# Optimization experiments

Hardware: AMD Instinct MI355X
Metric: run time of the kernel (lower is better)

Reference implementation:

```python
import jax, jax.numpy as jnp
import numpy as np

B, L, D_MODEL = 2, 4096, 1024
D_INNER = 2048  # expand * d_model
D_CONV = 4


def setup_inputs() -> dict:
    key = jax.random.key(0)
    ks = jax.random.split(key, 7)
    return {
        "hidden_states": jax.random.normal(ks[0], (B, L, D_MODEL), jnp.float32),
        "W_in": jax.random.normal(ks[1], (2 * D_INNER, D_MODEL), jnp.float32) * 0.02,
        "conv_w": jax.random.normal(ks[2], (D_INNER, D_CONV), jnp.float32) * 0.1,
        "conv_b": jax.random.normal(ks[3], (D_INNER,), jnp.float32) * 0.1,
        "k_ssm": jax.random.normal(ks[4], (D_INNER, L), jnp.float32) * 0.02,  # materialized SSM kernel (channels=1)
        "D_skip": jax.random.normal(ks[5], (D_INNER,), jnp.float32),
        "W_out": jax.random.normal(ks[6], (D_MODEL, D_INNER), jnp.float32) * 0.02,
    }


def _silu(x):
    return x * jax.nn.sigmoid(x)


def reference(hidden_states, W_in, conv_w, conv_b, k_ssm, D_skip, W_out):
    Bq, Lq, _ = hidden_states.shape
    # in_proj (no bias): (B, L, d_model) -> (B, 2*d_inner, L)
    xz = jnp.einsum('bld,ed->bel', hidden_states, W_in)
    x, z = jnp.split(xz, 2, axis=1)  # each (B, d_inner, L)

    # causal depthwise conv1d (pad left d_conv-1) + SiLU (causal_conv1d_fn)
    xp = jnp.pad(x, ((0, 0), (0, 0), (D_CONV - 1, 0)))
    xc = conv_b[None, :, None]
    for j in range(D_CONV):
        xc = xc + conv_w[None, :, j, None] * xp[:, :, j:j + Lq]
    x = _silu(xc)

    # FFT long convolution (l_kernel = L, n = 2L), channels = 1
    n = 2 * Lq
    x_f = jnp.fft.rfft(x, n=n)            # (B, H, n//2+1) complex
    k_f = jnp.fft.rfft(k_ssm, n=n)        # (H, n//2+1)
    y = jnp.fft.irfft(x_f * k_f[None], n=n)[..., :Lq]  # (B, H, L)

    # D skip connection
    y = y + x * D_skip[None, :, None]

    # gating with SiLU(z)
    y = y * _silu(z)

    # out_proj (no bias): (B, H, L) -> (B, L, d_model)
    return jnp.einsum('bhl,dh->bld', y, W_out)
```

## Files before the change

### kernel.cpp

```cpp
#include <hip/hip_runtime.h>
#include <hip/hip_bf16.h>
#include <math.h>

#define B_SZ 2
#define L_SZ 4096
#define DM   1024
#define DI   2048
#define E_SZ 4096
#define DC   4

typedef unsigned short u16;
typedef __attribute__((ext_vector_type(8))) short short8;
typedef __attribute__((ext_vector_type(4))) float f32x4;

__device__ __forceinline__ float silu_f(float v) {
    return v / (1.0f + __expf(-v));
}

__device__ __forceinline__ void split_bf16(float x, u16& h, u16& l) {
    unsigned u  = __float_as_uint(x);
    unsigned hb = u & 0xFFFF0000u;
    h = (u16)(hb >> 16);
    float lf = x - __uint_as_float(hb);
    l = (u16)(__float_as_uint(lf) >> 16);
}
__device__ __forceinline__ float bf2f(u16 h) {
    return __uint_as_float(((unsigned)h) << 16);
}

__device__ __forceinline__ void gld_lds16(const u16* g, u16* l) {
    __builtin_amdgcn_global_load_lds(
        (const __attribute__((address_space(1))) unsigned int*)g,
        (__attribute__((address_space(3))) unsigned int*)l, 16, 0, 0);
}

__global__ __launch_bounds__(256) void pack_rm(
    const float* __restrict__ X, u16* __restrict__ H, u16* __restrict__ Lo,
    int ldx, int r16n, long sX, long sOut)
{
    const long cid = (long)blockIdx.x * 256 + threadIdx.x;
    const int  qc  = (int)(cid & 63);
    const long blk = cid >> 6;
    const int  r16 = (int)(blk % r16n);
    const int  k32 = (int)(blk / r16n);
    const int  q = qc >> 4, m = qc & 15;

    const float* src = X + blockIdx.y * sX + (long)(r16 * 16 + m) * ldx + k32 * 32 + q * 8;
    float4 v0 = *(const float4*)src;
    float4 v1 = *(const float4*)(src + 4);
    float v[8] = {v0.x,v0.y,v0.z,v0.w,v1.x,v1.y,v1.z,v1.w};

    u16 hs[8], ls[8];
    #pragma unroll
    for (int j = 0; j < 8; ++j) split_bf16(v[j], hs[j], ls[j]);

    const long o = blockIdx.y * sOut + cid * 8;
    *(uint4*)&H[o]  = *(const uint4*)hs;
    *(uint4*)&Lo[o] = *(const uint4*)ls;
}

__global__ __launch_bounds__(256) void gemm_mfma(
    const u16* __restrict__ Ah, const u16* __restrict__ Al,
    const u16* __restrict__ Bh, const u16* __restrict__ Bl,
    float* __restrict__ C,
    int r16A, int r16B, long sA, long sB, long sC,
    int ldc, int nk32)
{
    __shared__ alignas(16) u16 sm[4][4096];

    const int tid  = threadIdx.x;
    const int wv   = tid >> 6, lane = tid & 63;
    const long zb  = blockIdx.z;

    const u16* srcs0 = Ah + zb * sA;
    const u16* srcs1 = Al + zb * sA;
    const u16* srcs2 = Bh + zb * sB;
    const u16* srcs3 = Bl + zb * sB;
    const u16* mysrc = (wv == 0) ? srcs0 : (wv == 1) ? srcs1 : (wv == 2) ? srcs2 : srcs3;
    const int  rblk  = (wv < 2) ? blockIdx.x * 8 : blockIdx.y * 8;
    const int  r16c  = (wv < 2) ? r16A : r16B;
    u16* myl = sm[wv];

    const int wr = wv >> 1, wc = wv & 1;

    f32x4 acc[4][4];
    #pragma unroll
    for (int i = 0; i < 4; ++i)
        #pragma unroll
        for (int j = 0; j < 4; ++j)
            #pragma unroll
            for (int r = 0; r < 4; ++r) acc[i][j][r] = 0.f;

    for (int s = 0; s < nk32; ++s) {
        if (s) __syncthreads();
        {
            const u16* g = mysrc + (((long)s * r16c + rblk) << 9) + lane * 8;
            #pragma unroll
            for (int i = 0; i < 8; ++i)
                gld_lds16(g + (i << 9), myl + (i << 9));
        }
        __syncthreads();

        short8 afh[4], afl[4], bfh[4], bfl[4];
        const int aoff = (wr * 4) * 512 + lane * 8;
        const int boff = (wc * 4) * 512 + lane * 8;
        #pragma unroll
        for (int t = 0; t < 4; ++t) {
            afh[t] = *(const short8*)&sm[0][aoff + t * 512];
            afl[t] = *(const short8*)&sm[1][aoff + t * 512];
            bfh[t] = *(const short8*)&sm[2][boff + t * 512];
            bfl[t] = *(const short8*)&sm[3][boff + t * 512];
        }
        #pragma unroll
        for (int i = 0; i < 4; ++i)
            #pragma unroll
            for (int j = 0; j < 4; ++j) {
                acc[i][j] = __builtin_amdgcn_mfma_f32_16x16x32_bf16(afh[i], bfh[j], acc[i][j], 0, 0, 0);
                acc[i][j] = __builtin_amdgcn_mfma_f32_16x16x32_bf16(afh[i], bfl[j], acc[i][j], 0, 0, 0);
                acc[i][j] = __builtin_amdgcn_mfma_f32_16x16x32_bf16(afl[i], bfh[j], acc[i][j], 0, 0, 0);
            }
    }

    const int m_ = lane & 15, q_ = lane >> 4;
    float* Cb = C + zb * sC;
    const int row00 = blockIdx.x * 128 + wr * 64 + q_ * 4;
    const int col0  = blockIdx.y * 128 + wc * 64 + m_;
    #pragma unroll
    for (int i = 0; i < 4; ++i)
        #pragma unroll
        for (int j = 0; j < 4; ++j) {
            const long base = (long)(row00 + i * 16) * ldc + col0 + j * 16;
            #pragma unroll
            for (int r = 0; r < 4; ++r)
                Cb[base + (long)r * ldc] = acc[i][j][r];
        }
}

__global__ __launch_bounds__(256) void conv_silu_split(
    const float* __restrict__ xz, const float* __restrict__ conv_w,
    const float* __restrict__ conv_b,
    u16* __restrict__ xh_gl, u16* __restrict__ xl_gl)
{
    const long gid = (long)blockIdx.x * 256 + threadIdx.x;
    const int  q   = (int)(gid % (L_SZ / 4));
    const long bc  = gid / (L_SZ / 4);
    const int  ch  = (int)(bc % DI);
    const int  b   = (int)(bc / DI);

    const float* row = xz + ((long)b * E_SZ + ch) * L_SZ;
    const int l0 = q * 4;

    float4 cur  = *(const float4*)&row[l0];
    float4 prev = q ? *(const float4*)&row[l0 - 4] : make_float4(0.f, 0.f, 0.f, 0.f);

    const float w0 = conv_w[ch*DC+0], w1 = conv_w[ch*DC+1];
    const float w2 = conv_w[ch*DC+2], w3 = conv_w[ch*DC+3];
    const float bias = conv_b[ch];

    float o[4];
    o[0] = silu_f(bias + w0*prev.y + w1*prev.z + w2*prev.w + w3*cur.x);
    o[1] = silu_f(bias + w0*prev.z + w1*prev.w + w2*cur.x  + w3*cur.y);
    o[2] = silu_f(bias + w0*prev.w + w1*cur.x  + w2*cur.y  + w3*cur.z);
    o[3] = silu_f(bias + w0*cur.x  + w1*cur.y  + w2*cur.z  + w3*cur.w);

    unsigned long long hp = 0ull, lp = 0ull;
    #pragma unroll
    for (int r = 0; r < 4; ++r) {
        u16 h, l; split_bf16(o[r], h, l);
        hp |= ((unsigned long long)h) << (16*r);
        lp |= ((unsigned long long)l) << (16*r);
    }
    const long base = ((long)b * DI + ch) * L_SZ + l0;
    *(unsigned long long*)&xh_gl[base] = hp;
    *(unsigned long long*)&xl_gl[base] = lp;
}

__global__ __launch_bounds__(256, 4) void longconv_mfma(
    u16* __restrict__ xh_gl, u16* __restrict__ xl_gl,
    const float* __restrict__ xz,  const float* __restrict__ k_ssm,
    const float* __restrict__ D_skip)
{
    __shared__ u16 XH[4352];
    __shared__ u16 XL[4352];

    const int tid  = threadIdx.x;
    const int lane = tid & 63;
    const int wv   = tid >> 6;
    const int wc   = blockIdx.x;
    const int ch   = wc & (DI - 1);
    const int b    = wc >> 11;

    u16*         xhr  = xh_gl + ((long)b * DI + ch) * L_SZ;
    u16*         xlr  = xl_gl + ((long)b * DI + ch) * L_SZ;
    const float* krow = k_ssm + (long)ch * L_SZ;

    if (tid < 64) {
        uint4 z = make_uint4(0u, 0u, 0u, 0u);
        ((uint4*)((tid < 32) ? XH : XL))[tid & 31] = z;
    }
    #pragma unroll
    for (int it = 0; it < 2; ++it) {
        const int idx = it * 256 + tid;
        *(uint4*)&XH[256 + idx * 8] = ((const uint4*)xhr)[idx];
        *(uint4*)&XL[256 + idx * 8] = ((const uint4*)xlr)[idx];
    }
    __syncthreads();

    const int m_ = lane & 15;
    const int q_ = lane >> 4;
    const int dq = m_ - 8 * q_ + ((q_ >= 2) ? 32 : 0);
    const int xoff_lane = 256 + 16 * m_ + 8 * q_ - ((q_ >= 2) ? 32 : 0);

    const int tset[4] = { wv, 7 - wv, 8 + wv, 15 - wv };
    const int tmax = 15 - wv;
    const int cmax = 8 * tmax + 7;

    f32x4 acc[4];
    #pragma unroll
    for (int u = 0; u < 4; ++u)
        #pragma unroll
        for (int r = 0; r < 4; ++r) acc[u][r] = 0.f;

    float kn[8];
    #pragma unroll
    for (int e = 0; e < 8; ++e) {
        const int ki = dq - e;
        kn[e] = (ki >= 0) ? krow[ki] : 0.0f;
    }

    for (int c = 0; c <= cmax; ++c) {
        float kv[8];
        #pragma unroll
        for (int e = 0; e < 8; ++e) kv[e] = kn[e];
        if (c < cmax) {
            #pragma unroll
            for (int e = 0; e < 8; ++e) {
                const int ki = 32 * (c + 1) + dq - e;
                kn[e] = (ki >= 0) ? krow[ki] : 0.0f;
            }
        }

        short8 ah, al;
        #pragma unroll
        for (int e = 0; e < 8; ++e) {
            u16 h, l; split_bf16(kv[e], h, l);
            ah[e] = (short)h; al[e] = (short)l;
        }

        const int xbase = xoff_lane - 32 * c;
        #pragma unroll
        for (int u = 0; u < 4; ++u) {
            const int t = tset[u];
            if (8 * t >= c - 7) {
                short8 bh = *(const short8*)&XH[xbase + 256 * t];
                short8 bl = *(const short8*)&XL[xbase + 256 * t];
                acc[u] = __builtin_amdgcn_mfma_f32_16x16x32_bf16(ah, bh, acc[u], 0, 0, 0);
                acc[u] = __builtin_amdgcn_mfma_f32_16x16x32_bf16(ah, bl, acc[u], 0, 0, 0);
                acc[u] = __builtin_amdgcn_mfma_f32_16x16x32_bf16(al, bh, acc[u], 0, 0, 0);
            }
        }
    }

    const float  Ds   = D_skip[ch];
    const float* zrow = xz + ((long)b * E_SZ + DI + ch) * L_SZ;

    #pragma unroll
    for (int u = 0; u < 4; ++u) {
        const int t  = tset[u];
        const int l0 = 256 * t + 16 * m_ + 4 * q_;
        float4 zv = *(const float4*)&zrow[l0];
        float zt[4] = { zv.x, zv.y, zv.z, zv.w };
        unsigned long long hp = 0ull, lp = 0ull;
        #pragma unroll
        for (int r = 0; r < 4; ++r) {
            const float xf = bf2f(XH[256 + l0 + r]) + bf2f(XL[256 + l0 + r]);
            const float o  = (acc[u][r] + Ds * xf) * silu_f(zt[r]);
            u16 h, l; split_bf16(o, h, l);
            hp |= ((unsigned long long)h) << (16*r);
            lp |= ((unsigned long long)l) << (16*r);
        }
        *(unsigned long long*)&xhr[l0] = hp;
        *(unsigned long long*)&xlr[l0] = lp;
    }
}

__global__ __launch_bounds__(256) void pack_y(
    const u16* __restrict__ Yh, const u16* __restrict__ Yl,
    u16* __restrict__ OH, u16* __restrict__ OL, long sOut)
{
    __shared__ u16 T[2][32][136];
    const int t  = threadIdx.x;
    const int l0 = blockIdx.x * 128;
    const int h0 = blockIdx.y * 32;
    const int b  = blockIdx.z;

    const u16* yb_h = Yh + ((long)b * DI + h0) * L_SZ + l0;
    const u16* yb_l = Yl + ((long)b * DI + h0) * L_SZ + l0;

    #pragma unroll
    for (int i = 0; i < 2; ++i) {
        const int c = t + 256 * i;
        const int row = c >> 4, col = (c & 15) * 8;
        *(uint4*)&T[0][row][col] = *(const uint4*)&yb_h[(long)row * L_SZ + col];
        *(uint4*)&T[1][row][col] = *(const uint4*)&yb_l[(long)row * L_SZ + col];
    }
    __syncthreads();

    u16* outs[2] = { OH + b * sOut, OL + b * sOut };
    #pragma unroll
    for (int p = 0; p < 2; ++p) {
        #pragma unroll
        for (int i = 0; i < 2; ++i) {
            const int c = t + 256 * i;
            const int r16b = c >> 6, qc = c & 63;
            const int q = qc >> 4, m = qc & 15;
            const int l = r16b * 16 + m;
            u16 vals[8];
            #pragma unroll
            for (int j = 0; j < 8; ++j) vals[j] = T[p][q * 8 + j][l];
            const long o = ((long)(blockIdx.y * 256 + blockIdx.x * 8 + r16b) << 9) + qc * 8;
            *(uint4*)&outs[p][o] = *(const uint4*)vals;
        }
    }
}

extern "C" void kernel_launch(void* const* d_in, const int* in_sizes, int n_in,
                              void* d_out, int out_size, void* d_ws, size_t ws_size,
                              hipStream_t stream)
{
    const float* hidden = (const float*)d_in[0];
    const float* W_in   = (const float*)d_in[1];
    const float* conv_w = (const float*)d_in[2];
    const float* conv_b = (const float*)d_in[3];
    const float* k_ssm  = (const float*)d_in[4];
    const float* D_skip = (const float*)d_in[5];
    const float* W_out  = (const float*)d_in[6];
    float* out = (float*)d_out;

    char* ws = (char*)d_ws;
    float* xz  = (float*)ws;
    u16*   xh  = (u16*)(ws + 134217728);
    u16*   xl  = (u16*)(ws + 167772160);
    u16*   WinH  = (u16*)(ws + 201326592);
    u16*   WinL  = WinH + 4194304;
    u16*   WoutH = (u16*)(ws + 201326592);
    u16*   WoutL = WoutH + 2097152;
    u16*   hidH  = (u16*)(ws + 218103808);
    u16*   hidL  = hidH + 8388608;
    u16*   yAh   = (u16*)ws;
    u16*   yAl   = yAh + 8388608;

    pack_rm<<<dim3(2048, 1), 256, 0, stream>>>(W_in, WinH, WinL, DM, 256, 0L, 0L);
    pack_rm<<<dim3(2048, B_SZ), 256, 0, stream>>>(hidden, hidH, hidL, DM, 256,
        (long)L_SZ * DM, 4194304L);

    gemm_mfma<<<dim3(32, 32, B_SZ), 256, 0, stream>>>(
        WinH, WinL, hidH, hidL, xz,
        256, 256, 0L, 4194304L, (long)E_SZ * L_SZ, L_SZ, 32);

    conv_silu_split<<<dim3((unsigned)((long)B_SZ*DI*(L_SZ/4)/256)), 256, 0, stream>>>(
        xz, conv_w, conv_b, xh, xl);

    longconv_mfma<<<dim3(B_SZ * DI), 256, 0, stream>>>(
        xh, xl, xz, k_ssm, D_skip);

    pack_rm<<<dim3(1024, 1), 256, 0, stream>>>(W_out, WoutH, WoutL, DI, 64, 0L, 0L);

    pack_y<<<dim3(32, 64, B_SZ), 256, 0, stream>>>(
        xh, xl, yAh, yAl, 33554432L);

    gemm_mfma<<<dim3(32, 8, B_SZ), 256, 0, stream>>>(
        yAh, yAl, WoutH, WoutL, out,
        256, 64, 33554432L, 0L, (long)L_SZ * DM, DM, 64);
}
```

Baseline: 635.3 us.

## Pre-split SSM kernel into packed bf16 hi/lo and load X directly to LDS

Adds a pack_k kernel that splits k_ssm once into interleaved bf16 hi/lo words, so the long-conv inner loop builds its MFMA A operands with byte permutes instead of redoing the float split every iteration for every batch. The X tile staging switches to direct global-to-LDS loads, and the occupancy hint rises from 4 to 6 blocks. The packed k buffer reuses workspace space already consumed by the conv stage, at the cost of one extra launch and pass over k_ssm. Higher occupancy may limit registers and cause spills.

New measurement: 622.6 us. 1.02x faster.

```diff
diff --git a/kernel.cpp b/kernel.cpp
--- a/kernel.cpp
+++ b/kernel.cpp
@@ -175,13 +175,32 @@
     *(unsigned long long*)&xl_gl[base] = lp;
 }
 
-__global__ __launch_bounds__(256, 4) void longconv_mfma(
+__global__ __launch_bounds__(256) void pack_k(
+    const float* __restrict__ k_ssm, unsigned* __restrict__ kv)
+{
+    const long gid = (long)blockIdx.x * 256 + threadIdx.x;
+    const int  qq  = (int)(gid & (L_SZ / 4 - 1));
+    const int  ch  = (int)(gid >> 10);
+
+    const long off = ((long)ch << 12) + qq * 4;
+    float4 v = *(const float4*)&k_ssm[off];
+    float f[4] = { v.x, v.y, v.z, v.w };
+    unsigned o[4];
+    #pragma unroll
+    for (int r = 0; r < 4; ++r) {
+        u16 h, l; split_bf16(f[r], h, l);
+        o[r] = (unsigned)h | ((unsigned)l << 16);
+    }
+    *(uint4*)&kv[off] = *(const uint4*)o;
+}
+
+__global__ __launch_bounds__(256, 6) void longconv_mfma(
     u16* __restrict__ xh_gl, u16* __restrict__ xl_gl,
-    const float* __restrict__ xz,  const float* __restrict__ k_ssm,
+    const float* __restrict__ xz,  const unsigned* __restrict__ kv,
     const float* __restrict__ D_skip)
 {
-    __shared__ u16 XH[4352];
-    __shared__ u16 XL[4352];
+    __shared__ alignas(16) u16 XH[4352];
+    __shared__ alignas(16) u16 XL[4352];
 
     const int tid  = threadIdx.x;
     const int lane = tid & 63;
@@ -190,19 +209,20 @@
     const int ch   = wc & (DI - 1);
     const int b    = wc >> 11;
 
-    u16*         xhr  = xh_gl + ((long)b * DI + ch) * L_SZ;
-    u16*         xlr  = xl_gl + ((long)b * DI + ch) * L_SZ;
-    const float* krow = k_ssm + (long)ch * L_SZ;
+    u16*            xhr = xh_gl + ((long)b * DI + ch) * L_SZ;
+    u16*            xlr = xl_gl + ((long)b * DI + ch) * L_SZ;
+    const unsigned* kvr = kv + ((long)ch << 12);
 
     if (tid < 64) {
         uint4 z = make_uint4(0u, 0u, 0u, 0u);
         ((uint4*)((tid < 32) ? XH : XL))[tid & 31] = z;
     }
-    #pragma unroll
-    for (int it = 0; it < 2; ++it) {
-        const int idx = it * 256 + tid;
-        *(uint4*)&XH[256 + idx * 8] = ((const uint4*)xhr)[idx];
-        *(uint4*)&XL[256 + idx * 8] = ((const uint4*)xlr)[idx];
+    {
+        const int ck = wv * 2;
+        gld_lds16(xhr + (ck    ) * 512 + lane * 8, XH + 256 + (ck    ) * 512);
+        gld_lds16(xhr + (ck + 1) * 512 + lane * 8, XH + 256 + (ck + 1) * 512);
+        gld_lds16(xlr + (ck    ) * 512 + lane * 8, XL + 256 + (ck    ) * 512);
+        gld_lds16(xlr + (ck + 1) * 512 + lane * 8, XL + 256 + (ck + 1) * 512);
     }
     __syncthreads();
 
@@ -221,30 +241,29 @@
         #pragma unroll
         for (int r = 0; r < 4; ++r) acc[u][r] = 0.f;
 
-    float kn[8];
+    const unsigned* kp = kvr + dq;
+
+    unsigned lcur[8];
     #pragma unroll
     for (int e = 0; e < 8; ++e) {
         const int ki = dq - e;
-        kn[e] = (ki >= 0) ? krow[ki] : 0.0f;
+        lcur[e] = (ki >= 0) ? kvr[ki] : 0u;
     }
 
     for (int c = 0; c <= cmax; ++c) {
-        float kv[8];
-        #pragma unroll
-        for (int e = 0; e < 8; ++e) kv[e] = kn[e];
+        union { unsigned u[4]; short8 s; } Ah_, Al_;
+        #pragma unroll
+        for (int i = 0; i < 4; ++i) {
+            Ah_.u[i] = __builtin_amdgcn_perm(lcur[2*i+1], lcur[2*i], 0x05040100u);
+            Al_.u[i] = __builtin_amdgcn_perm(lcur[2*i+1], lcur[2*i], 0x07060302u);
+        }
+        const short8 ah = Ah_.s, al = Al_.s;
+
+        unsigned lnext[8];
         if (c < cmax) {
-            #pragma unroll
-            for (int e = 0; e < 8; ++e) {
-                const int ki = 32 * (c + 1) + dq - e;
-                kn[e] = (ki >= 0) ? krow[ki] : 0.0f;
-            }
-        }
-
-        short8 ah, al;
-        #pragma unroll
-        for (int e = 0; e < 8; ++e) {
-            u16 h, l; split_bf16(kv[e], h, l);
-            ah[e] = (short)h; al[e] = (short)l;
+            const int kb = 32 * (c + 1);
+            #pragma unroll
+            for (int e = 0; e < 8; ++e) lnext[e] = kp[kb - e];
         }
 
         const int xbase = xoff_lane - 32 * c;
@@ -258,6 +277,11 @@
                 acc[u] = __builtin_amdgcn_mfma_f32_16x16x32_bf16(ah, bl, acc[u], 0, 0, 0);
                 acc[u] = __builtin_amdgcn_mfma_f32_16x16x32_bf16(al, bh, acc[u], 0, 0, 0);
             }
+        }
+
+        if (c < cmax) {
+            #pragma unroll
+            for (int e = 0; e < 8; ++e) lcur[e] = lnext[e];
         }
     }
 
@@ -347,6 +371,7 @@
     u16*   WoutL = WoutH + 2097152;
     u16*   hidH  = (u16*)(ws + 218103808);
     u16*   hidL  = hidH + 8388608;
+    unsigned* klv = (unsigned*)ws;
     u16*   yAh   = (u16*)ws;
     u16*   yAl   = yAh + 8388608;
 
@@ -361,8 +386,10 @@
     conv_silu_split<<<dim3((unsigned)((long)B_SZ*DI*(L_SZ/4)/256)), 256, 0, stream>>>(
         xz, conv_w, conv_b, xh, xl);
 
+    pack_k<<<dim3((unsigned)((long)DI * (L_SZ/4) / 256)), 256, 0, stream>>>(k_ssm, klv);
+
     longconv_mfma<<<dim3(B_SZ * DI), 256, 0, stream>>>(
-        xh, xl, xz, k_ssm, D_skip);
+        xh, xl, xz, klv, D_skip);
 
     pack_rm<<<dim3(1024, 1), 256, 0, stream>>>(W_out, WoutH, WoutL, DI, 64, 0L, 0L);
 
```
